# Kernel tuning notes

Measured on AMD Instinct MI355X. Metric: run time of the kernel, lower is better.

Reference implementation:

```python
import jax, jax.numpy as jnp
import numpy as np

N = 50000
E = 800000
HID = 128


def _gat_conv(x, src, dst, W, al, ar, b, n):
    # DGL GATConv, num_heads=1, negative_slope=0.2, bias=True
    z = x @ W                                  # [N, F]
    el = z @ al                                # [N]
    er = z @ ar                                # [N]
    e = jax.nn.leaky_relu(el[src] + er[dst], 0.2)   # [E]
    m = jax.ops.segment_max(e, dst, num_segments=n)  # per-dst max for stable softmax
    ex = jnp.exp(e - m[dst])
    denom = jax.ops.segment_sum(ex, dst, num_segments=n)
    alpha = ex / (denom[dst] + 1e-9)           # edge softmax over incoming edges
    out = jax.ops.segment_sum(alpha[:, None] * z[src], dst, num_segments=n)
    return out + b


def setup_inputs() -> dict:
    key = jax.random.key(0)
    ks = jax.random.split(key, 16)
    inp = {
        "x": jax.random.normal(ks[0], (N, 2), jnp.float32),
        "src": jax.random.randint(ks[1], (E,), 0, N, jnp.int32),
        "dst": jax.random.randint(ks[2], (E,), 0, N, jnp.int32),
        "W1": jax.random.normal(ks[3], (2, HID), jnp.float32) * 0.5,
        "al1": jax.random.normal(ks[4], (HID,), jnp.float32) * 0.1,
        "ar1": jax.random.normal(ks[5], (HID,), jnp.float32) * 0.1,
        "b1": jnp.zeros((HID,), jnp.float32),
        "W2": jax.random.normal(ks[6], (HID, HID), jnp.float32) * (1.0 / np.sqrt(HID)),
        "al2": jax.random.normal(ks[7], (HID,), jnp.float32) * 0.1,
        "ar2": jax.random.normal(ks[8], (HID,), jnp.float32) * 0.1,
        "b2": jnp.zeros((HID,), jnp.float32),
        "Wlin": jax.random.normal(ks[9], (HID, 3), jnp.float32) * (1.0 / np.sqrt(HID)),
        "blin": jnp.zeros((3,), jnp.float32),
        "alpha0": jnp.float32(1.0),
        "beta0": jnp.float32(1.0),
        "gamma0": jnp.float32(1.0),
        "dt": jnp.float32(0.5),
    }
    return inp


def reference(x, src, dst, W1, al1, ar1, b1, W2, al2, ar2, b2, Wlin, blin,
              alpha0, beta0, gamma0, dt):
    h = _gat_conv(x, src, dst, W1, al1, ar1, b1, N)
    h = jax.nn.relu(h)
    h = _gat_conv(h, src, dst, W2, al2, ar2, b2, N)
    h = jax.nn.relu(h)
    h = jax.nn.sigmoid(h @ Wlin + blin)        # [N, 3]
    # (original computes unsplice/splice predictions from alpha0/beta0/gamma0/dt
    #  but does not return them; returned value is the mean over rate channels)
    return h.mean(axis=-1)                     # [N]


if __name__ == "__main__":
    out = reference(**setup_inputs())
    print(out.shape, out.dtype)
```

## Files before the change

kernel.cpp:

```cpp
#include <hip/hip_runtime.h>
#include <math.h>

#define NN 50000
#define EE 800000
#define HIDF 128
#define NPAD 50176

#define BSHIFT 9
#define BKTN 98
#define BCAP 10000

typedef unsigned int uint;
typedef unsigned short ushort;
typedef unsigned char uchar;
typedef short bf16x8 __attribute__((ext_vector_type(8)));
typedef float f32x4 __attribute__((ext_vector_type(4)));
typedef float f32x2 __attribute__((ext_vector_type(2)));

__device__ inline ushort bf16_rtne(float x) {
  uint u = __float_as_uint(x);
  return (ushort)((u + 0x7fffu + ((u >> 16) & 1u)) >> 16);
}
__device__ inline uint pack2_bf16(float a, float b) {
  return (uint)bf16_rtne(a) | ((uint)bf16_rtne(b) << 16);
}
__device__ inline float rdlanef(float p, int jj) {
  return __uint_as_float(__builtin_amdgcn_readlane(__float_as_uint(p), jj));
}
__device__ inline float lo16(uint z) { return __uint_as_float(z << 16); }
__device__ inline float hi16(uint z) { return __uint_as_float(z & 0xffff0000u); }

__global__ void k_prep(const float* __restrict__ W1, const float* __restrict__ al1,
                       const float* __restrict__ ar1,
                       const float* __restrict__ W2, const float* __restrict__ al2,
                       const float* __restrict__ ar2,
                       ushort* __restrict__ Bfrag, float* __restrict__ wel,
                       float* __restrict__ wer, float* __restrict__ params,
                       int* __restrict__ bcnt) {
  int b = blockIdx.x, tid = threadIdx.x;
  if (b < 16) {
    int e = b * 1024 + tid * 4;
#pragma unroll
    for (int q = 0; q < 4; ++q, ++e) {
      int k = e >> 7, n = e & 127;
      float v = W2[e];
      ushort hi = bf16_rtne(v);
      ushort lo = bf16_rtne(v - __uint_as_float((uint)hi << 16));
      int g = n >> 4, t = k >> 5;
      int l = (n & 15) | (((k >> 3) & 3) << 4);
      int j = k & 7;
      int idx = ((g * 4 + t) * 64 + l) * 8 + j;
      Bfrag[idx] = hi;
      Bfrag[16384 + idx] = lo;
    }
  } else {
    if (tid < BKTN) bcnt[tid] = 0;
    if (tid < 128) {
      float acc = 0.f;
      for (int k = 0; k < 128; ++k) acc += W2[k * 128 + tid] * al2[k];
      wel[tid] = acc;
    } else {
      int n = tid - 128;
      float acc = 0.f;
      for (int k = 0; k < 128; ++k) acc += W2[k * 128 + n] * ar2[k];
      wer[n] = acc;
    }
    if (tid < 4) {
      const float* vec = (tid & 2) ? ar1 : al1;
      const float* wrow = W1 + (tid & 1) * HIDF;
      float acc = 0.f;
      for (int f = 0; f < HIDF; ++f) acc += wrow[f] * vec[f];
      params[tid] = acc;
    }
  }
}

__global__ __launch_bounds__(256) void k_binA(const int* __restrict__ src,
                                              const int* __restrict__ dst,
                                              int* __restrict__ bcnt, uint* __restrict__ bcoo) {
  __shared__ uint stage[4096];
  __shared__ uchar stageb[4096];
  __shared__ int bh[BKTN], bbase[BKTN], gbase[BKTN], lcur[BKTN];
  __shared__ int sc[128];
  int tid = threadIdx.x;
  int e0 = blockIdx.x * 4096;
  int nE = min(4096, EE - e0);
  if (tid < BKTN) bh[tid] = 0;
  __syncthreads();

  int myb[16];
  uint myv[16];
#pragma unroll
  for (int k = 0; k < 16; ++k) {
    int i = e0 + k * 256 + tid;
    myb[k] = -1;
    if (i < EE) {
      int s = src[i], d = dst[i];
      myb[k] = d >> BSHIFT;
      myv[k] = ((uint)s << BSHIFT) | (uint)(d & 511);
      atomicAdd(&bh[myb[k]], 1);
    }
  }
  __syncthreads();

  {
    int v = (tid < BKTN) ? bh[tid] : 0;
    if (tid < 128) sc[tid] = v;
    __syncthreads();
    for (int o = 1; o < 128; o <<= 1) {
      int add = (tid >= o && tid < 128) ? sc[tid - o] : 0;
      __syncthreads();
      if (tid < 128) sc[tid] += add;
      __syncthreads();
    }
    if (tid < BKTN) {
      int excl = sc[tid] - bh[tid];
      bbase[tid] = excl;
      lcur[tid] = excl;
      gbase[tid] = atomicAdd(&bcnt[tid], bh[tid]);
    }
  }
  __syncthreads();

#pragma unroll
  for (int k = 0; k < 16; ++k) {
    if (myb[k] >= 0) {
      int slot = atomicAdd(&lcur[myb[k]], 1);
      stage[slot] = myv[k];
      stageb[slot] = (uchar)myb[k];
    }
  }
  __syncthreads();

  for (int s2 = tid; s2 < nE; s2 += 256) {
    int b = stageb[s2];
    bcoo[(size_t)b * BCAP + gbase[b] + (s2 - bbase[b])] = stage[s2];
  }
}

__global__ __launch_bounds__(256) void k_binB(const uint* __restrict__ bcoo,
                                              const int* __restrict__ bcnt,
                                              int* __restrict__ rowp, int* __restrict__ srcs) {
  __shared__ int h[512], pref[512], ps[256];
  __shared__ int basebuf;
  int b = blockIdx.x, tid = threadIdx.x;
  int cnt = bcnt[b];

  {
    int v = (tid < BKTN) ? bcnt[tid] : 0;
    if (tid < 128) ps[tid] = v;
    __syncthreads();
    for (int o = 1; o < 128; o <<= 1) {
      int add = (tid >= o && tid < 128) ? ps[tid - o] : 0;
      __syncthreads();
      if (tid < 128) ps[tid] += add;
      __syncthreads();
    }
    if (tid == 0) {
      basebuf = (b == 0) ? 0 : ps[b - 1];
      if (b == 0) rowp[NN] = EE;
    }
  }
  h[tid] = 0;
  h[tid + 256] = 0;
  __syncthreads();
  int base = basebuf;
  const uint* mc = bcoo + (size_t)b * BCAP;
  for (int i = tid; i < cnt; i += 256) atomicAdd(&h[mc[i] & 511], 1);
  __syncthreads();
  int a0 = h[2 * tid], a1 = h[2 * tid + 1];
  int s = a0 + a1;
  ps[tid] = s;
  __syncthreads();
  for (int o = 1; o < 256; o <<= 1) {
    int add = (tid >= o) ? ps[tid - o] : 0;
    __syncthreads();
    ps[tid] += add;
    __syncthreads();
  }
  int excl = ps[tid] - s;
  pref[2 * tid] = excl;
  pref[2 * tid + 1] = excl + a0;
  __syncthreads();
  int n0 = b << BSHIFT;
  for (int j = tid; j < 512; j += 256)
    if (n0 + j < NN) rowp[n0 + j] = base + pref[j];
  __syncthreads();
  for (int i = tid; i < cnt; i += 256) {
    uint v = mc[i];
    int pos = atomicAdd(&pref[v & 511], 1);
    srcs[base + pos] = (int)(v >> BSHIFT);
  }
}

__global__ void k_agg1(const int* __restrict__ rowp, const int* __restrict__ srcs,
                       const float* __restrict__ x, const float* __restrict__ params,
                       const float* __restrict__ W1, const float* __restrict__ b1,
                       ushort* __restrict__ Hhi, ushort* __restrict__ Hlo,
                       const float* __restrict__ wel, const float* __restrict__ wer,
                       float* __restrict__ el2, float* __restrict__ er2) {
  int v = blockIdx.x * 4 + (threadIdx.x >> 6);
  if (v >= NN) return;
  int lane = threadIdx.x & 63;
  float wl1x = params[0], wl1y = params[1], wr1x = params[2], wr1y = params[3];
  float2 xv = ((const float2*)x)[v];
  float erv = fmaf(xv.x, wr1x, xv.y * wr1y);
  int beg = rowp[v], end = rowp[v + 1];

  float psum = 0.f, ax = 0.f, ay = 0.f;
  for (int j = beg + lane; j < end; j += 64) {
    int s = srcs[j];
    float2 xs = ((const float2*)x)[s];
    float t = fmaf(xs.x, wl1x, xs.y * wl1y) + erv;
    t = fmaxf(t, 0.2f * t);
    float p = __expf(t);
    psum += p;
    ax = fmaf(p, xs.x, ax);
    ay = fmaf(p, xs.y, ay);
  }
  for (int o = 32; o; o >>= 1) {
    psum += __shfl_xor(psum, o);
    ax += __shfl_xor(ax, o);
    ay += __shfl_xor(ay, o);
  }
  float inv = 1.0f / (psum + 1e-9f);
  ax *= inv;
  ay *= inv;

  float2 w0 = ((const float2*)W1)[lane];
  float2 w1 = ((const float2*)(W1 + HIDF))[lane];
  float2 bv = ((const float2*)b1)[lane];
  float ox = fmaxf(fmaf(ax, w0.x, fmaf(ay, w1.x, bv.x)), 0.f);
  float oy = fmaxf(fmaf(ax, w0.y, fmaf(ay, w1.y, bv.y)), 0.f);

  ushort hx = bf16_rtne(ox), hy = bf16_rtne(oy);
  ((uint*)Hhi)[(size_t)v * 64 + lane] = (uint)hx | ((uint)hy << 16);
  float lx = ox - __uint_as_float((uint)hx << 16);
  float ly = oy - __uint_as_float((uint)hy << 16);
  ((uint*)Hlo)[(size_t)v * 64 + lane] = pack2_bf16(lx, ly);
  float2 wl = ((const float2*)wel)[lane];
  float2 wr = ((const float2*)wer)[lane];
  float ep = ox * wl.x + oy * wl.y;
  float rp = ox * wr.x + oy * wr.y;
  for (int o = 32; o; o >>= 1) {
    ep += __shfl_xor(ep, o);
    rp += __shfl_xor(rp, o);
  }
  if (lane == 0) { el2[v] = ep; er2[v] = rp; }
}

__global__ __launch_bounds__(256) void k_gemm_mfma(
    const ushort* __restrict__ Hhi, const ushort* __restrict__ Hlo,
    const ushort* __restrict__ Bfrag, ushort* __restrict__ z) {
  int tid = threadIdx.x;
  int lane = tid & 63;
  int wid = tid >> 6;
  int base = blockIdx.x * 128;

  bf16x8 bhi[2][4], blo[2][4];
  const bf16x8* bp = (const bf16x8*)Bfrag;
#pragma unroll
  for (int gi = 0; gi < 2; ++gi)
#pragma unroll
    for (int t = 0; t < 4; ++t) {
      int idx = ((wid * 2 + gi) * 4 + t) * 64 + lane;
      bhi[gi][t] = bp[idx];
      blo[gi][t] = bp[2048 + idx];
    }

  int arow = lane & 15;
  int koff = (lane >> 4) * 8;
  const bf16x8* ahp = (const bf16x8*)(Hhi + (size_t)(base + arow) * HIDF + koff);
  const bf16x8* alp = (const bf16x8*)(Hlo + (size_t)(base + arow) * HIDF + koff);

  bf16x8 ah[4], av[4];
#pragma unroll
  for (int t = 0; t < 4; ++t) { ah[t] = ahp[t * 4]; av[t] = alp[t * 4]; }

#pragma unroll
  for (int mt = 0; mt < 8; ++mt) {
    bf16x8 nah[4], nav[4];
#pragma unroll
    for (int t = 0; t < 4; ++t) { nah[t] = ah[t]; nav[t] = av[t]; }
    if (mt < 7) {
#pragma unroll
      for (int t = 0; t < 4; ++t) {
        nah[t] = ahp[(mt + 1) * 256 + t * 4];
        nav[t] = alp[(mt + 1) * 256 + t * 4];
      }
    }
    f32x4 c0a = {0.f, 0.f, 0.f, 0.f}, c0b = {0.f, 0.f, 0.f, 0.f};
    f32x4 c1a = {0.f, 0.f, 0.f, 0.f}, c1b = {0.f, 0.f, 0.f, 0.f};
#pragma unroll
    for (int t = 0; t < 4; ++t) {
      f32x4& c0 = (t & 1) ? c0b : c0a;
      f32x4& c1 = (t & 1) ? c1b : c1a;
      c0 = __builtin_amdgcn_mfma_f32_16x16x32_bf16(ah[t], bhi[0][t], c0, 0, 0, 0);
      c1 = __builtin_amdgcn_mfma_f32_16x16x32_bf16(ah[t], bhi[1][t], c1, 0, 0, 0);
      c0 = __builtin_amdgcn_mfma_f32_16x16x32_bf16(ah[t], blo[0][t], c0, 0, 0, 0);
      c1 = __builtin_amdgcn_mfma_f32_16x16x32_bf16(ah[t], blo[1][t], c1, 0, 0, 0);
      c0 = __builtin_amdgcn_mfma_f32_16x16x32_bf16(av[t], bhi[0][t], c0, 0, 0, 0);
      c1 = __builtin_amdgcn_mfma_f32_16x16x32_bf16(av[t], bhi[1][t], c1, 0, 0, 0);
    }
    f32x4 c0 = c0a + c0b;
    f32x4 c1 = c1a + c1b;
    int r0 = base + mt * 16 + (lane >> 4) * 4;
    int cc = wid * 32 + (lane & 15);
    ushort* zp = z + (size_t)r0 * HIDF + cc;
#pragma unroll
    for (int i = 0; i < 4; ++i) {
      zp[i * HIDF] = bf16_rtne(c0[i]);
      zp[i * HIDF + 16] = bf16_rtne(c1[i]);
    }
#pragma unroll
    for (int t = 0; t < 4; ++t) { ah[t] = nah[t]; av[t] = nav[t]; }
  }
}

#define PAIR(JJ)                                                        \
  {                                                                     \
    float pA = rdlanef(p, (JJ)), pB = rdlanef(p, (JJ) + 1);             \
    int sA = __builtin_amdgcn_readlane(s, (JJ));                        \
    int sB = __builtin_amdgcn_readlane(s, (JJ) + 1);                    \
    uint zA = zl[(uint)sA * 64u];                                       \
    uint zB = zl[(uint)sB * 64u];                                       \
    f32x2 vA = {lo16(zA), hi16(zA)};                                    \
    f32x2 vB = {lo16(zB), hi16(zB)};                                    \
    acc = vA * (f32x2){pA, pA} + acc;                                   \
    acc = vB * (f32x2){pB, pB} + acc;                                   \
  }

__global__ void k_agg2(const int* __restrict__ rowp, const int* __restrict__ srcs,
                       const float* __restrict__ el, const float* __restrict__ er,
                       const ushort* __restrict__ z, const float* __restrict__ bias,
                       float* __restrict__ out,
                       const float* __restrict__ Wlin, const float* __restrict__ blin) {
  int v = blockIdx.x * 4 + (threadIdx.x >> 6);
  if (v >= NN) return;
  int lane = threadIdx.x & 63;
  int beg = rowp[v], end = rowp[v + 1];
  float erv = er[v];
  float psum = 0.f;
  f32x2 acc = {0.f, 0.f};
  const uint* zl = (const uint*)z + lane;

  for (int cb = beg; cb < end; cb += 64) {
    int j = cb + lane;
    int s = srcs[min(j, end - 1)];
    float t = el[s] + erv;
    t = fmaxf(t, 0.2f * t);
    float p = (j < end) ? __expf(t) : 0.f;
    psum += p;
    int cnt = min(64, end - cb);
    int bb = 0;
    for (; bb + 16 <= cnt; bb += 16) {
#pragma unroll
      for (int u = 0; u < 16; u += 2) PAIR(bb + u)
    }
    for (; bb < cnt; bb += 2) PAIR(bb)
  }

  float denom = psum;
  for (int o = 32; o; o >>= 1) denom += __shfl_xor(denom, o);
  float inv = 1.0f / (denom + 1e-9f);
  float2 bv = ((const float2*)bias)[lane];
  float ox = fmaxf(fmaf(acc.x, inv, bv.x), 0.f);
  float oy = fmaxf(fmaf(acc.y, inv, bv.y), 0.f);

  int f0 = lane * 2;
  const float* w0 = &Wlin[f0 * 3];
  float d0 = fmaf(ox, w0[0], oy * w0[3]);
  float d1 = fmaf(ox, w0[1], oy * w0[4]);
  float d2 = fmaf(ox, w0[2], oy * w0[5]);
  for (int o = 32; o; o >>= 1) {
    d0 += __shfl_xor(d0, o);
    d1 += __shfl_xor(d1, o);
    d2 += __shfl_xor(d2, o);
  }
  if (lane == 0) {
    float s0 = 1.f / (1.f + __expf(-(d0 + blin[0])));
    float s1 = 1.f / (1.f + __expf(-(d1 + blin[1])));
    float s2 = 1.f / (1.f + __expf(-(d2 + blin[2])));
    out[v] = (s0 + s1 + s2) * (1.f / 3.f);
  }
}

extern "C" void kernel_launch(void* const* d_in, const int* in_sizes, int n_in,
                              void* d_out, int out_size, void* d_ws, size_t ws_size,
                              hipStream_t stream) {
  const float* x    = (const float*)d_in[0];
  const int*   src  = (const int*)d_in[1];
  const int*   dst  = (const int*)d_in[2];
  const float* W1   = (const float*)d_in[3];
  const float* al1  = (const float*)d_in[4];
  const float* ar1  = (const float*)d_in[5];
  const float* b1   = (const float*)d_in[6];
  const float* W2   = (const float*)d_in[7];
  const float* al2  = (const float*)d_in[8];
  const float* ar2  = (const float*)d_in[9];
  const float* b2   = (const float*)d_in[10];
  const float* Wlin = (const float*)d_in[11];
  const float* blin = (const float*)d_in[12];
  float* out = (float*)d_out;

  char* ws = (char*)d_ws;
  size_t off = 0;
  auto alloc = [&](size_t bytes) -> char* {
    char* p = ws + off;
    off += (bytes + 255) & ~(size_t)255;
    return p;
  };
  int*    rowp   = (int*)alloc((size_t)(NN + 1) * 4);
  int*    srcs   = (int*)alloc((size_t)EE * 4);
  int*    bcnt   = (int*)alloc(BKTN * 4);
  uint*   bcoo   = (uint*)alloc((size_t)BKTN * BCAP * 4);
  float*  el2    = (float*)alloc((size_t)NN * 4);
  float*  er2    = (float*)alloc((size_t)NN * 4);
  float*  wel    = (float*)alloc(HIDF * 4);
  float*  wer    = (float*)alloc(HIDF * 4);
  float*  params = (float*)alloc(16 * 4);
  ushort* Bfrag  = (ushort*)alloc(2 * 16384 * 2);
  ushort* Z      = (ushort*)alloc((size_t)NPAD * HIDF * 2);
  ushort* Hhi    = (ushort*)alloc((size_t)NPAD * HIDF * 2);
  ushort* Hlo    = (ushort*)alloc((size_t)NPAD * HIDF * 2);

  const int nbNode4 = (NN + 3) / 4;
  const int nbGemm = (NN + 127) / 128;
  const int nbBinA = (EE + 4095) / 4096;

  k_prep<<<17, 256, 0, stream>>>(W1, al1, ar1, W2, al2, ar2,
                                 Bfrag, wel, wer, params, bcnt);

  k_binA<<<nbBinA, 256, 0, stream>>>(src, dst, bcnt, bcoo);
  k_binB<<<BKTN, 256, 0, stream>>>(bcoo, bcnt, rowp, srcs);

  k_agg1<<<nbNode4, 256, 0, stream>>>(rowp, srcs, x, params, W1, b1,
                                      Hhi, Hlo, wel, wer, el2, er2);

  k_gemm_mfma<<<nbGemm, 256, 0, stream>>>(Hhi, Hlo, Bfrag, Z);
  k_agg2<<<nbNode4, 256, 0, stream>>>(rowp, srcs, el2, er2, Z, b2, out, Wlin, blin);
}
```

Measured before the change: 120.9 us.

## Quantize layer-2 features to int8 per row for the edge gather

Adds a kernel that quantizes each row of the bf16 projected features Z to int8 with a per-row absmax scale. The scale is stored next to el in a float2 array, so the softmax logit and the dequant scale come from a single load. The aggregation kernel then gathers 2 bytes per lane instead of 4 and folds the scale into the attention weight. The aim is to halve the dominant random-gather traffic over 800k edges. In exchange it adds an extra kernel pass over Z and lowers accuracy to int8, which may breach tolerance.

```diff
diff --git a/kernel.cpp b/kernel.cpp
--- a/kernel.cpp
+++ b/kernel.cpp
@@ -198,7 +198,7 @@
                        const float* __restrict__ W1, const float* __restrict__ b1,
                        ushort* __restrict__ Hhi, ushort* __restrict__ Hlo,
                        const float* __restrict__ wel, const float* __restrict__ wer,
-                       float* __restrict__ el2, float* __restrict__ er2) {
+                       float2* __restrict__ els, float* __restrict__ er2) {
   int v = blockIdx.x * 4 + (threadIdx.x >> 6);
   if (v >= NN) return;
   int lane = threadIdx.x & 63;
@@ -246,7 +246,7 @@
     ep += __shfl_xor(ep, o);
     rp += __shfl_xor(rp, o);
   }
-  if (lane == 0) { el2[v] = ep; er2[v] = rp; }
+  if (lane == 0) { els[v].x = ep; er2[v] = rp; }
 }
 
 __global__ __launch_bounds__(256) void k_gemm_mfma(
@@ -317,22 +317,40 @@
   }
 }
 
-#define PAIR(JJ)                                                        \
+__global__ void k_quant(const ushort* __restrict__ Z, ushort* __restrict__ q8,
+                        float2* __restrict__ els) {
+  int v = blockIdx.x * 4 + (threadIdx.x >> 6);
+  if (v >= NN) return;
+  int lane = threadIdx.x & 63;
+  uint zz = ((const uint*)Z)[(size_t)v * 64 + lane];
+  float a = lo16(zz), b = hi16(zz);
+  float m = fmaxf(fabsf(a), fabsf(b));
+  for (int o = 32; o; o >>= 1) m = fmaxf(m, __shfl_xor(m, o));
+  float inv = (m > 0.f) ? 127.f / m : 0.f;
+  int qa = __float2int_rn(a * inv);
+  int qb = __float2int_rn(b * inv);
+  q8[(size_t)v * 64 + lane] = (ushort)((qa & 0xff) | ((qb & 0xff) << 8));
+  if (lane == 0) els[v].y = m * (1.f / 127.f);
+}
+
+#define PAIRQ(JJ)                                                       \
   {                                                                     \
-    float pA = rdlanef(p, (JJ)), pB = rdlanef(p, (JJ) + 1);             \
+    float psA = rdlanef(ps, (JJ)), psB = rdlanef(ps, (JJ) + 1);         \
     int sA = __builtin_amdgcn_readlane(s, (JJ));                        \
     int sB = __builtin_amdgcn_readlane(s, (JJ) + 1);                    \
-    uint zA = zl[(uint)sA * 64u];                                       \
-    uint zB = zl[(uint)sB * 64u];                                       \
-    f32x2 vA = {lo16(zA), hi16(zA)};                                    \
-    f32x2 vB = {lo16(zB), hi16(zB)};                                    \
-    acc = vA * (f32x2){pA, pA} + acc;                                   \
-    acc = vB * (f32x2){pB, pB} + acc;                                   \
+    uint qA = (uint)q8l[(size_t)sA * 64u];                              \
+    uint qB = (uint)q8l[(size_t)sB * 64u];                              \
+    f32x2 vA = {(float)(int)(char)(qA & 0xff),                          \
+                (float)(int)(char)((qA >> 8) & 0xff)};                  \
+    f32x2 vB = {(float)(int)(char)(qB & 0xff),                          \
+                (float)(int)(char)((qB >> 8) & 0xff)};                  \
+    acc = vA * (f32x2){psA, psA} + acc;                                 \
+    acc = vB * (f32x2){psB, psB} + acc;                                 \
   }
 
 __global__ void k_agg2(const int* __restrict__ rowp, const int* __restrict__ srcs,
-                       const float* __restrict__ el, const float* __restrict__ er,
-                       const ushort* __restrict__ z, const float* __restrict__ bias,
+                       const float2* __restrict__ els, const float* __restrict__ er,
+                       const ushort* __restrict__ q8, const float* __restrict__ bias,
                        float* __restrict__ out,
                        const float* __restrict__ Wlin, const float* __restrict__ blin) {
   int v = blockIdx.x * 4 + (threadIdx.x >> 6);
@@ -342,22 +360,24 @@
   float erv = er[v];
   float psum = 0.f;
   f32x2 acc = {0.f, 0.f};
-  const uint* zl = (const uint*)z + lane;
+  const ushort* q8l = q8 + lane;
 
   for (int cb = beg; cb < end; cb += 64) {
     int j = cb + lane;
     int s = srcs[min(j, end - 1)];
-    float t = el[s] + erv;
+    float2 es = els[s];
+    float t = es.x + erv;
     t = fmaxf(t, 0.2f * t);
     float p = (j < end) ? __expf(t) : 0.f;
     psum += p;
+    float ps = p * es.y;
     int cnt = min(64, end - cb);
     int bb = 0;
     for (; bb + 16 <= cnt; bb += 16) {
 #pragma unroll
-      for (int u = 0; u < 16; u += 2) PAIR(bb + u)
-    }
-    for (; bb < cnt; bb += 2) PAIR(bb)
+      for (int u = 0; u < 16; u += 2) PAIRQ(bb + u)
+    }
+    for (; bb < cnt; bb += 2) PAIRQ(bb)
   }
 
   float denom = psum;
@@ -414,13 +434,14 @@
   int*    srcs   = (int*)alloc((size_t)EE * 4);
   int*    bcnt   = (int*)alloc(BKTN * 4);
   uint*   bcoo   = (uint*)alloc((size_t)BKTN * BCAP * 4);
-  float*  el2    = (float*)alloc((size_t)NN * 4);
+  float2* els    = (float2*)alloc((size_t)NN * 8);
   float*  er2    = (float*)alloc((size_t)NN * 4);
   float*  wel    = (float*)alloc(HIDF * 4);
   float*  wer    = (float*)alloc(HIDF * 4);
   float*  params = (float*)alloc(16 * 4);
   ushort* Bfrag  = (ushort*)alloc(2 * 16384 * 2);
   ushort* Z      = (ushort*)alloc((size_t)NPAD * HIDF * 2);
+  ushort* Q8     = (ushort*)alloc((size_t)NPAD * HIDF);
   ushort* Hhi    = (ushort*)alloc((size_t)NPAD * HIDF * 2);
   ushort* Hlo    = (ushort*)alloc((size_t)NPAD * HIDF * 2);
 
@@ -435,8 +456,9 @@
   k_binB<<<BKTN, 256, 0, stream>>>(bcoo, bcnt, rowp, srcs);
 
   k_agg1<<<nbNode4, 256, 0, stream>>>(rowp, srcs, x, params, W1, b1,
-                                      Hhi, Hlo, wel, wer, el2, er2);
+                                      Hhi, Hlo, wel, wer, els, er2);
 
   k_gemm_mfma<<<nbGemm, 256, 0, stream>>>(Hhi, Hlo, Bfrag, Z);
-  k_agg2<<<nbNode4, 256, 0, stream>>>(rowp, srcs, el2, er2, Z, b2, out, Wlin, blin);
-}
+  k_quant<<<nbNode4, 256, 0, stream>>>(Z, Q8, els);
+  k_agg2<<<nbNode4, 256, 0, stream>>>(rowp, srcs, els, er2, Q8, b2, out, Wlin, blin);
+}
```

Result: slower. 127.5 us (+5.5%).

## Split Z into feature quarters and aggregate per quarter with XCC-affine work queues

Applied to the files above, without the earlier changes.

The GEMM now writes Z as four 32-column slabs, so each quarter (about 3.2 MB) can stay resident in one XCD's L2. A new persistent aggregation kernel reads the XCC id and starts on a matching quarter, pulling 64-node chunks from per-quarter atomic counters. The softmax denominator moves into a separate k_denom pass, and partial Wlin dot products from each quarter go to a buffer that a final kernel reduces and passes through sigmoid. The aim is to cut L2 misses on the random gather of Z, at the cost of two extra launches, recomputing exp per quarter, and extra global traffic for the partial outputs.

```diff
diff --git a/kernel.cpp b/kernel.cpp
--- a/kernel.cpp
+++ b/kernel.cpp
@@ -9,6 +9,7 @@
 #define BSHIFT 9
 #define BKTN 98
 #define BCAP 10000
+#define NCH 782
 
 typedef unsigned int uint;
 typedef unsigned short ushort;
@@ -24,9 +25,6 @@
 __device__ inline uint pack2_bf16(float a, float b) {
   return (uint)bf16_rtne(a) | ((uint)bf16_rtne(b) << 16);
 }
-__device__ inline float rdlanef(float p, int jj) {
-  return __uint_as_float(__builtin_amdgcn_readlane(__float_as_uint(p), jj));
-}
 __device__ inline float lo16(uint z) { return __uint_as_float(z << 16); }
 __device__ inline float hi16(uint z) { return __uint_as_float(z & 0xffff0000u); }
 
@@ -36,7 +34,7 @@
                        const float* __restrict__ ar2,
                        ushort* __restrict__ Bfrag, float* __restrict__ wel,
                        float* __restrict__ wer, float* __restrict__ params,
-                       int* __restrict__ bcnt) {
+                       int* __restrict__ bcnt, int* __restrict__ qctr) {
   int b = blockIdx.x, tid = threadIdx.x;
   if (b < 16) {
     int e = b * 1024 + tid * 4;
@@ -55,6 +53,7 @@
     }
   } else {
     if (tid < BKTN) bcnt[tid] = 0;
+    if (tid < 4) qctr[tid] = 0;
     if (tid < 128) {
       float acc = 0.f;
       for (int k = 0; k < 128; ++k) acc += W2[k * 128 + tid] * al2[k];
@@ -305,84 +304,114 @@
     f32x4 c0 = c0a + c0b;
     f32x4 c1 = c1a + c1b;
     int r0 = base + mt * 16 + (lane >> 4) * 4;
-    int cc = wid * 32 + (lane & 15);
-    ushort* zp = z + (size_t)r0 * HIDF + cc;
+    ushort* zp = z + (size_t)wid * NPAD * 32 + (size_t)r0 * 32 + (lane & 15);
 #pragma unroll
     for (int i = 0; i < 4; ++i) {
-      zp[i * HIDF] = bf16_rtne(c0[i]);
-      zp[i * HIDF + 16] = bf16_rtne(c1[i]);
+      zp[i * 32] = bf16_rtne(c0[i]);
+      zp[i * 32 + 16] = bf16_rtne(c1[i]);
     }
 #pragma unroll
     for (int t = 0; t < 4; ++t) { ah[t] = nah[t]; av[t] = nav[t]; }
   }
 }
 
-#define PAIR(JJ)                                                        \
-  {                                                                     \
-    float pA = rdlanef(p, (JJ)), pB = rdlanef(p, (JJ) + 1);             \
-    int sA = __builtin_amdgcn_readlane(s, (JJ));                        \
-    int sB = __builtin_amdgcn_readlane(s, (JJ) + 1);                    \
-    uint zA = zl[(uint)sA * 64u];                                       \
-    uint zB = zl[(uint)sB * 64u];                                       \
-    f32x2 vA = {lo16(zA), hi16(zA)};                                    \
-    f32x2 vB = {lo16(zB), hi16(zB)};                                    \
-    acc = vA * (f32x2){pA, pA} + acc;                                   \
-    acc = vB * (f32x2){pB, pB} + acc;                                   \
-  }
-
-__global__ void k_agg2(const int* __restrict__ rowp, const int* __restrict__ srcs,
-                       const float* __restrict__ el, const float* __restrict__ er,
-                       const ushort* __restrict__ z, const float* __restrict__ bias,
-                       float* __restrict__ out,
-                       const float* __restrict__ Wlin, const float* __restrict__ blin) {
+__global__ void k_denom(const int* __restrict__ rowp, const int* __restrict__ srcs,
+                        const float* __restrict__ el2, const float* __restrict__ er2,
+                        float* __restrict__ invd) {
   int v = blockIdx.x * 4 + (threadIdx.x >> 6);
   if (v >= NN) return;
   int lane = threadIdx.x & 63;
   int beg = rowp[v], end = rowp[v + 1];
-  float erv = er[v];
-  float psum = 0.f;
-  f32x2 acc = {0.f, 0.f};
-  const uint* zl = (const uint*)z + lane;
-
-  for (int cb = beg; cb < end; cb += 64) {
-    int j = cb + lane;
-    int s = srcs[min(j, end - 1)];
-    float t = el[s] + erv;
+  float erv = er2[v];
+  float ps = 0.f;
+  for (int j = beg + lane; j < end; j += 64) {
+    float t = el2[srcs[j]] + erv;
     t = fmaxf(t, 0.2f * t);
-    float p = (j < end) ? __expf(t) : 0.f;
-    psum += p;
-    int cnt = min(64, end - cb);
-    int bb = 0;
-    for (; bb + 16 <= cnt; bb += 16) {
-#pragma unroll
-      for (int u = 0; u < 16; u += 2) PAIR(bb + u)
-    }
-    for (; bb < cnt; bb += 2) PAIR(bb)
-  }
-
-  float denom = psum;
-  for (int o = 32; o; o >>= 1) denom += __shfl_xor(denom, o);
-  float inv = 1.0f / (denom + 1e-9f);
-  float2 bv = ((const float2*)bias)[lane];
-  float ox = fmaxf(fmaf(acc.x, inv, bv.x), 0.f);
-  float oy = fmaxf(fmaf(acc.y, inv, bv.y), 0.f);
-
-  int f0 = lane * 2;
-  const float* w0 = &Wlin[f0 * 3];
-  float d0 = fmaf(ox, w0[0], oy * w0[3]);
-  float d1 = fmaf(ox, w0[1], oy * w0[4]);
-  float d2 = fmaf(ox, w0[2], oy * w0[5]);
-  for (int o = 32; o; o >>= 1) {
-    d0 += __shfl_xor(d0, o);
-    d1 += __shfl_xor(d1, o);
-    d2 += __shfl_xor(d2, o);
-  }
-  if (lane == 0) {
-    float s0 = 1.f / (1.f + __expf(-(d0 + blin[0])));
-    float s1 = 1.f / (1.f + __expf(-(d1 + blin[1])));
-    float s2 = 1.f / (1.f + __expf(-(d2 + blin[2])));
-    out[v] = (s0 + s1 + s2) * (1.f / 3.f);
-  }
+    ps += __expf(t);
+  }
+  for (int o = 32; o; o >>= 1) ps += __shfl_xor(ps, o);
+  if (lane == 0) invd[v] = 1.0f / (ps + 1e-9f);
+}
+
+__global__ __launch_bounds__(256) void k_aggx(
+    const int* __restrict__ rowp, const int* __restrict__ srcs,
+    const float* __restrict__ el2, const float* __restrict__ er2,
+    const float* __restrict__ invd, const ushort* __restrict__ Zq,
+    const float* __restrict__ b2, const float* __restrict__ Wlin,
+    float* __restrict__ out3q, int* __restrict__ qctr) {
+  __shared__ int chunkS;
+  int tid = threadIdx.x;
+  int wid = tid >> 6;
+  int lane = tid & 63;
+  int g = lane >> 4, li = lane & 15;
+  uint xcc = __builtin_amdgcn_s_getreg(6164);
+  int q0 = (int)(xcc & 3u);
+
+  for (int t = 0; t < 4; ++t) {
+    int q = (q0 + t) & 3;
+    const uint* Zu = (const uint*)Zq + (size_t)q * NPAD * 16;
+    int f0 = q * 32 + li * 2;
+    float b0 = b2[f0], b1v = b2[f0 + 1];
+    const float* w0 = &Wlin[f0 * 3];
+    float w00 = w0[0], w01 = w0[1], w02 = w0[2];
+    float w10 = w0[3], w11 = w0[4], w12 = w0[5];
+    while (true) {
+      __syncthreads();
+      if (tid == 0) chunkS = atomicAdd(&qctr[q], 1);
+      __syncthreads();
+      int c = chunkS;
+      if (c >= NCH) break;
+      int vbase = c * 64 + wid * 16;
+      for (int nn = 0; nn < 16; ++nn) {
+        int v = vbase + nn;
+        if (v >= NN) break;
+        int beg = rowp[v], end = rowp[v + 1];
+        float erv = er2[v];
+        f32x2 acc = {0.f, 0.f};
+        for (int jj = beg; jj < end; jj += 4) {
+          int j = jj + g;
+          int s = srcs[min(j, end - 1)];
+          float tt = el2[s] + erv;
+          tt = fmaxf(tt, 0.2f * tt);
+          float p = (j < end) ? __expf(tt) : 0.f;
+          uint zz = Zu[(uint)s * 16u + (uint)li];
+          acc += (f32x2){lo16(zz), hi16(zz)} * (f32x2){p, p};
+        }
+        float a0 = acc.x, a1 = acc.y;
+        a0 += __shfl_xor(a0, 16); a0 += __shfl_xor(a0, 32);
+        a1 += __shfl_xor(a1, 16); a1 += __shfl_xor(a1, 32);
+        float inv = invd[v];
+        float ox = fmaxf(fmaf(a0, inv, b0), 0.f);
+        float oy = fmaxf(fmaf(a1, inv, b1v), 0.f);
+        float d0 = fmaf(ox, w00, oy * w10);
+        float d1 = fmaf(ox, w01, oy * w11);
+        float d2 = fmaf(ox, w02, oy * w12);
+        for (int o = 8; o; o >>= 1) {
+          d0 += __shfl_xor(d0, o);
+          d1 += __shfl_xor(d1, o);
+          d2 += __shfl_xor(d2, o);
+        }
+        if (lane == 0) {
+          out3q[(size_t)(q * 3 + 0) * NN + v] = d0;
+          out3q[(size_t)(q * 3 + 1) * NN + v] = d1;
+          out3q[(size_t)(q * 3 + 2) * NN + v] = d2;
+        }
+      }
+    }
+  }
+}
+
+__global__ void k_final(const float* __restrict__ out3q, const float* __restrict__ blin,
+                        float* __restrict__ out) {
+  int v = blockIdx.x * 256 + threadIdx.x;
+  if (v >= NN) return;
+  float d0 = out3q[v] + out3q[3 * (size_t)NN + v] + out3q[6 * (size_t)NN + v] + out3q[9 * (size_t)NN + v];
+  float d1 = out3q[(size_t)NN + v] + out3q[4 * (size_t)NN + v] + out3q[7 * (size_t)NN + v] + out3q[10 * (size_t)NN + v];
+  float d2 = out3q[2 * (size_t)NN + v] + out3q[5 * (size_t)NN + v] + out3q[8 * (size_t)NN + v] + out3q[11 * (size_t)NN + v];
+  float s0 = 1.f / (1.f + __expf(-(d0 + blin[0])));
+  float s1 = 1.f / (1.f + __expf(-(d1 + blin[1])));
+  float s2 = 1.f / (1.f + __expf(-(d2 + blin[2])));
+  out[v] = (s0 + s1 + s2) * (1.f / 3.f);
 }
 
 extern "C" void kernel_launch(void* const* d_in, const int* in_sizes, int n_in,
@@ -413,23 +442,27 @@
   int*    rowp   = (int*)alloc((size_t)(NN + 1) * 4);
   int*    srcs   = (int*)alloc((size_t)EE * 4);
   int*    bcnt   = (int*)alloc(BKTN * 4);
+  int*    qctr   = (int*)alloc(64);
   uint*   bcoo   = (uint*)alloc((size_t)BKTN * BCAP * 4);
   float*  el2    = (float*)alloc((size_t)NN * 4);
   float*  er2    = (float*)alloc((size_t)NN * 4);
+  float*  invd   = (float*)alloc((size_t)NN * 4);
+  float*  out3q  = (float*)alloc((size_t)NN * 12 * 4);
   float*  wel    = (float*)alloc(HIDF * 4);
   float*  wer    = (float*)alloc(HIDF * 4);
   float*  params = (float*)alloc(16 * 4);
   ushort* Bfrag  = (ushort*)alloc(2 * 16384 * 2);
-  ushort* Z      = (ushort*)alloc((size_t)NPAD * HIDF * 2);
+  ushort* Zq     = (ushort*)alloc((size_t)NPAD * HIDF * 2);
   ushort* Hhi    = (ushort*)alloc((size_t)NPAD * HIDF * 2);
   ushort* Hlo    = (ushort*)alloc((size_t)NPAD * HIDF * 2);
 
   const int nbNode4 = (NN + 3) / 4;
   const int nbGemm = (NN + 127) / 128;
   const int nbBinA = (EE + 4095) / 4096;
+  const int nbN = (NN + 255) / 256;
 
   k_prep<<<17, 256, 0, stream>>>(W1, al1, ar1, W2, al2, ar2,
-                                 Bfrag, wel, wer, params, bcnt);
+                                 Bfrag, wel, wer, params, bcnt, qctr);
 
   k_binA<<<nbBinA, 256, 0, stream>>>(src, dst, bcnt, bcoo);
   k_binB<<<BKTN, 256, 0, stream>>>(bcoo, bcnt, rowp, srcs);
@@ -437,6 +470,9 @@
   k_agg1<<<nbNode4, 256, 0, stream>>>(rowp, srcs, x, params, W1, b1,
                                       Hhi, Hlo, wel, wer, el2, er2);
 
-  k_gemm_mfma<<<nbGemm, 256, 0, stream>>>(Hhi, Hlo, Bfrag, Z);
-  k_agg2<<<nbNode4, 256, 0, stream>>>(rowp, srcs, el2, er2, Z, b2, out, Wlin, blin);
-}
+  k_gemm_mfma<<<nbGemm, 256, 0, stream>>>(Hhi, Hlo, Bfrag, Zq);
+  k_denom<<<nbNode4, 256, 0, stream>>>(rowp, srcs, el2, er2, invd);
+  k_aggx<<<2048, 256, 0, stream>>>(rowp, srcs, el2, er2, invd, Zq, b2, Wlin,
+                                   out3q, qctr);
+  k_final<<<nbN, 256, 0, stream>>>(out3q, blin, out);
+}
```

Result: slower. 292.3 us (+141.9%).
